# Kernel optimization log

Measured on AMD Instinct MI355X. Metric: run time of the kernel, lower is better.

## Reference

```python
import jax, jax.numpy as jnp
import numpy as np

B, S, DIM = 20, 500, 300          # hard-coded in the original module
HID = 600                          # expansion_factor * dim
QK = 128
ROT = 32                           # rotary dim = min(32, query_key_dim)
NB = 32                            # t5 num_buckets


def _layernorm(x, g, b, eps=1e-5):
    m = jnp.mean(x, -1, keepdims=True)
    v = jnp.var(x, -1, keepdims=True)
    return (x - m) / jnp.sqrt(v + eps) * g + b


def _silu(x):
    return x * jax.nn.sigmoid(x)


def _rotary(x):
    # rotate first ROT dims, adjacent-pair convention (rotary_embedding_torch)
    inv = 1.0 / (10000.0 ** (jnp.arange(0, ROT, 2, dtype=jnp.float32) / ROT))  # [16]
    fr = jnp.repeat(jnp.arange(S, dtype=jnp.float32)[:, None] * inv[None, :], 2, axis=-1)  # [S,32]
    cos, sin = jnp.cos(fr), jnp.sin(fr)
    xr, xp = x[..., :ROT], x[..., ROT:]
    x2 = xr.reshape(xr.shape[0], S, ROT // 2, 2)
    rot = jnp.stack([-x2[..., 1], x2[..., 0]], axis=-1).reshape(xr.shape)
    return jnp.concatenate([xr * cos + rot * sin, xp], axis=-1)


def _t5_bias(emb):
    nb = NB // 2                   # non-causal halves the buckets -> 16
    pos = jnp.arange(S)
    n = pos[:, None] - pos[None, :]  # n = -(k_pos - q_pos)
    ret = (n < 0).astype(jnp.int32) * nb
    na = jnp.abs(n)
    max_exact = nb // 2            # 8
    vil = max_exact + (jnp.log(jnp.maximum(na, 1).astype(jnp.float32) / max_exact)
                       / np.float32(np.log(128.0 / max_exact)) * (nb - max_exact)).astype(jnp.int32)
    vil = jnp.minimum(vil, nb - 1)
    bucket = ret + jnp.where(na < max_exact, na, vil)
    return emb[bucket, 0] * np.float32(QK ** 0.5)


def _gate_mask(gate):
    # Vectorized, jit-able version of the per-batch numpy threshold search.
    T = 128
    absg = jnp.abs(gate)                                   # [B,500,600]
    # histogram of floor(|g|): count(|g|>=t) for integer t via reverse cumsum
    bins = jnp.clip(jnp.floor(absg), 0, T).astype(jnp.int32)
    flat = (bins + (jnp.arange(B, dtype=jnp.int32) * (T + 1))[:, None, None]).ravel()
    hist = jnp.zeros(B * (T + 1), jnp.int32).at[flat].add(1).reshape(B, T + 1)
    cge = jnp.cumsum(hist[:, ::-1], axis=1)[:, ::-1]       # cge[:,t] = #(|g| >= t)
    gmax = jnp.floor(jnp.max(gate, axis=(1, 2)))           # loop starts at floor(max(gate))
    ts = jnp.arange(1, T + 1)
    valid = (ts[None, :] <= gmax[:, None]) & (cge[:, 1:] > 90000)  # 300000*0.3
    trim = jnp.maximum(jnp.max(jnp.where(valid, ts[None, :], 0), axis=1), 1)  # [B]
    g4 = absg.reshape(B, 100, 5, 120, 5)[:, :, :4, :, :4]
    counts = jnp.sum(g4 >= trim[:, None, None, None, None].astype(gate.dtype),
                     axis=(2, 4)).astype(jnp.int32)        # [B,100,120], <=16
    cmax = jnp.max(counts, axis=(1, 2))
    ts2 = jnp.arange(1, 17)
    c2 = jnp.sum(counts[:, :, :, None] >= ts2[None, None, None, :], axis=(1, 2))  # [B,16]
    valid2 = (ts2[None, :] <= cmax[:, None]) & (c2 > 3600)  # 12000*0.3
    found = jnp.any(valid2, axis=1)
    t2 = jnp.where(found, jnp.max(jnp.where(valid2, ts2[None, :], 0), axis=1), cmax)
    bv = jnp.where(counts >= t2[:, None, None], 1.0, 0.25).astype(gate.dtype)  # [B,100,120]
    pr = jnp.array([1.0, 1.0, 1.0, 1.0, 0.0], gate.dtype)  # 5th row/col of each block stays 0
    m = bv[:, :, None, :, None] * pr[None, None, :, None, None] * pr[None, None, None, None, :]
    return m.reshape(B, 500, 600)


def setup_inputs() -> dict:
    key = jax.random.key(0)
    ks = jax.random.split(key, 12)
    std = 0.02
    return {
        "x": jax.random.normal(ks[0], (B, S, DIM), jnp.float32),
        "my_mask2": jax.random.uniform(ks[1], (S, S), jnp.float32),
        "ln_g": jnp.ones((DIM,), jnp.float32),
        "ln_b": jnp.zeros((DIM,), jnp.float32),
        "Wh": jax.random.normal(ks[2], (DIM, 2 * HID), jnp.float32) * std,
        "bh": jnp.zeros((2 * HID,), jnp.float32),
        "Wqk": jax.random.normal(ks[3], (DIM, QK), jnp.float32) * std,
        "bqk": jnp.zeros((QK,), jnp.float32),
        "gamma": 1.0 + jax.random.normal(ks[4], (2, QK), jnp.float32) * std,
        "beta": jnp.zeros((2, QK), jnp.float32),
        "rel_emb": jax.random.normal(ks[5], (NB, 1), jnp.float32) * std,
        "Wout": jax.random.normal(ks[6], (HID, DIM), jnp.float32) * std,
        "bout": jnp.zeros((DIM,), jnp.float32),
    }


def reference(x, my_mask2, ln_g, ln_b, Wh, bh, Wqk, bqk, gamma, beta, rel_emb, Wout, bout):
    nx = _layernorm(x, ln_g, ln_b)
    xs, xp = nx[..., :DIM // 2], nx[..., DIM // 2:]
    xs = jnp.concatenate([jnp.zeros_like(xs[:, :1]), xs[:, :-1]], axis=1)  # token shift
    nx = jnp.concatenate([xs, xp], axis=-1)
    h = _silu(nx @ Wh + bh)                                 # [B,S,1200]
    v, gate = h[..., :HID], h[..., HID:]
    gm = jax.lax.stop_gradient(_gate_mask(gate))            # numpy path detaches in torch
    qk = _silu(nx @ Wqk + bqk)
    q = _rotary(qk * gamma[0] + beta[0])
    k = _rotary(qk * gamma[1] + beta[1])
    sim = jnp.einsum('bid,bjd->bij', q, k) + _t5_bias(rel_emb)[None]
    attn = jax.nn.relu(sim / S) ** 2
    attn = attn * my_mask2[None]
    out = jnp.einsum('bij,bjd->bid', attn, v)
    out = gm * out * gate
    return out @ Wout + bout + x
```

## Files before the change

### kernel.cpp

```cpp
#include <hip/hip_runtime.h>
#include <hip/hip_bf16.h>

#define BB 20
#define SS 500
#define DIMD 300
#define HIDH 600
#define QKD 128

typedef unsigned short u16;
typedef __attribute__((ext_vector_type(8))) __bf16 bf16x8;
typedef __attribute__((ext_vector_type(8))) short short8;
typedef __attribute__((ext_vector_type(4))) float floatx4;

__device__ __forceinline__ u16 f2bu(float f) {
    __hip_bfloat16 h = __float2bfloat16(f);
    return *reinterpret_cast<u16*>(&h);
}
__device__ __forceinline__ float bu2f(u16 u) {
    unsigned v = ((unsigned)u) << 16;
    return __uint_as_float(v);
}

__device__ __forceinline__ floatx4 mfma_bf16(short8 a, short8 b, floatx4 c) {
    return __builtin_amdgcn_mfma_f32_16x16x32_bf16(
        __builtin_bit_cast(bf16x8, a), __builtin_bit_cast(bf16x8, b), c, 0, 0, 0);
}

__device__ __forceinline__ void glds16(const u16* g, u16* l) {
    __builtin_amdgcn_global_load_lds(
        (__attribute__((address_space(1))) const void*)g,
        (__attribute__((address_space(3))) void*)l, 16, 0, 0);
}

__device__ __forceinline__ unsigned fenc(float m) {
    unsigned bits = __float_as_uint(m);
    return (bits & 0x80000000u) ? ~bits : (bits | 0x80000000u);
}

__global__ __launch_bounds__(256)
void prep_ln_kernel(const float* __restrict__ x, const float* __restrict__ lng,
                    const float* __restrict__ lnb, u16* __restrict__ nxb,
                    const float* __restrict__ Wh, const float* __restrict__ Wqk,
                    const float* __restrict__ Wout, const float* __restrict__ rel_emb,
                    u16* __restrict__ WhT, u16* __restrict__ Wqkb,
                    u16* __restrict__ WoutT, float* __restrict__ bias,
                    int* __restrict__ hist, unsigned* __restrict__ gmaxu,
                    int* __restrict__ h2cm) {
    long id = (long)blockIdx.x * 256 + threadIdx.x;
    if (id < 640000) {
        int bs = id >> 6;
        int t = id & 63;
        int s = bs % SS;
        const float* xr = x + (long)bs * DIMD;
        float sum = 0.f, sq = 0.f;
        for (int d = t; d < DIMD; d += 64) { float v = xr[d]; sum += v; sq += v * v; }
        for (int off = 1; off < 64; off <<= 1) {
            sum += __shfl_xor(sum, off);
            sq  += __shfl_xor(sq, off);
        }
        float mean = sum * (1.f / DIMD);
        float var  = sq * (1.f / DIMD) - mean * mean;
        float rstd = rsqrtf(var + 1e-5f);
        for (int d = t; d < DIMD; d += 64) {
            float nv = (xr[d] - mean) * rstd * lng[d] + lnb[d];
            if (d < DIMD / 2) {
                if (s < SS - 1) nxb[(long)(bs + 1) * 320 + d] = f2bu(nv);
            } else {
                nxb[(long)bs * 320 + d] = f2bu(nv);
            }
        }
        if (s == 0)
            for (int d = t; d < DIMD / 2; d += 64) nxb[(long)bs * 320 + d] = 0;
        for (int d = DIMD + t; d < 320; d += 64) nxb[(long)bs * 320 + d] = 0;
        return;
    }
    id -= 640000;
    if (id < 384000) {
        int k = id / 1200, n = id - (long)k * 1200;
        WhT[(long)n * 320 + k] = (k < 300) ? f2bu(Wh[(long)k * 1200 + n]) : (u16)0;
        return;
    }
    id -= 384000;
    if (id < 40960) {
        int k = id / 128, n = id - (long)k * 128;
        Wqkb[(long)n * 320 + k] = (k < 300) ? f2bu(Wqk[(long)k * 128 + n]) : (u16)0;
        return;
    }
    id -= 40960;
    if (id < 182400) {
        int k = id / 300, n = id - (long)k * 300;
        WoutT[(long)n * 608 + k] = (k < 600) ? f2bu(Wout[(long)k * 300 + n]) : (u16)0;
        return;
    }
    id -= 182400;
    if (id < 250000) {
        int i = id / 500, j = id - (long)i * 500;
        int n = i - j;
        int ret = (n < 0) ? 16 : 0;
        int na = n < 0 ? -n : n;
        int bucket;
        if (na < 8) bucket = ret + na;
        else {
            int vil = 8 + (int)(logf((float)na * 0.125f) / logf(16.f) * 8.f);
            vil = vil < 15 ? vil : 15;
            bucket = ret + vil;
        }
        bias[id] = rel_emb[bucket] * 11.313708498984761f;
        return;
    }
    id -= 250000;
    if (id < 5120) { hist[id] = 0; return; }
    id -= 5120;
    if (id < 1280) { gmaxu[id] = 0u; return; }
    id -= 1280;
    if (id < 1280) h2cm[(int)id] = 0;
}


struct EpiH {
    const float* bh; u16* vT; float* gateT; int* hist; unsigned* gmaxu;
    float gm0 = -1e30f, gm1 = -1e30f;
    __device__ void init(int) {}
    __device__ void operator()(float acc, int bz, int m, int n, int j) {
        if (m >= 1200 || n >= 10000) return;
        float v = acc + bh[m];
        v = v / (1.f + expf(-v));
        int b = n / SS, s = n - b * SS;
        if (m < HIDH) { vT[((long)b * 640 + m) * 512 + s] = f2bu(v); return; }
        gateT[((long)b * HIDH + (m - HIDH)) * SS + s] = v;
        if (j) gm1 = fmaxf(gm1, v); else gm0 = fmaxf(gm0, v);
        float ag = fabsf(v);
        if (ag >= 1.f) {
            int bin = (int)fminf(floorf(ag), 128.f);
            atomicAdd(&hist[b * 256 + bin], 1);
        }
    }
    __device__ void flushS(float m, int base) {
        if (base >= 10000) return;
        m = fmaxf(m, __shfl_xor(m, 16));
        m = fmaxf(m, __shfl_xor(m, 32));
        int b0 = base / SS;
        if (b0 == (base + 15) / SS) {
            m = fmaxf(m, __shfl_xor(m, 1));
            m = fmaxf(m, __shfl_xor(m, 2));
            m = fmaxf(m, __shfl_xor(m, 4));
            m = fmaxf(m, __shfl_xor(m, 8));
            if ((threadIdx.x & 63) == 0 && m > -1e29f)
                atomicMax(&gmaxu[b0 * 64], fenc(m));
        } else {
            int l = threadIdx.x & 63;
            if (l < 16 && m > -1e29f)
                atomicMax(&gmaxu[((base + l) / SS) * 64], fenc(m));
        }
    }
    __device__ void finish(int bz, int m0, int n0) {
        if (m0 + 32 <= 600) return;
        flushS(gm0, n0);
        flushS(gm1, n0 + 16);
    }
};
struct EpiQKRot {
    const float* bqk; const float* gamma; const float* beta;
    u16* qb; u16* kb;
    __device__ void init(int) const {}
    __device__ void operator()(float acc, int bz, int m, int n, int j) const {
        float v = acc + bqk[n];
        v = v / (1.f + expf(-v));
        float qp = v * gamma[n] + beta[n];
        float kp = v * gamma[QKD + n] + beta[QKD + n];
        float qx = __shfl_xor(qp, 1);
        float kx = __shfl_xor(kp, 1);
        float qo = qp, ko = kp;
        if (n < 32) {
            int s = m % SS;
            float inv = expf(-(float)(n & ~1) * (logf(10000.f) / 32.f));
            float ang = (float)s * inv;
            float c, sn;
            sincosf(ang, &sn, &c);
            float qr = (n & 1) ? qx : -qx;
            float kr = (n & 1) ? kx : -kx;
            qo = qp * c + qr * sn;
            ko = kp * c + kr * sn;
        }
        if (m < 10000) {
            qb[(long)m * QKD + n] = f2bu(qo);
            kb[(long)m * QKD + n] = f2bu(ko);
        }
    }
    __device__ void finish(int, int, int) const {}
};
struct EpiAttnB {
    const float* bias; const float* mask; u16* attnb;
    __device__ void init(int) const {}
    __device__ void operator()(float acc, int b, int m, int n, int j) const {
        if (m >= SS || n >= 512) return;
        float r = 0.f;
        if (n < SS) {
            float s = (acc + bias[m * SS + n]) * (1.f / (float)SS);
            s = fmaxf(s, 0.f);
            r = s * s * mask[m * SS + n];
        }
        attnb[((long)b * SS + m) * 512 + n] = f2bu(r);
    }
    __device__ void finish(int, int, int) const {}
};
struct EpiGateN {
    const float* gateT; const int* counts; const int* h2cm; u16* gated;
    int t2 = 0;
    __device__ void init(int b) {
        int cmax = h2cm[640 + b * 32];
        int suffix = 0, best = 0;
        bool found = false;
        for (int tt = 16; tt >= 1; --tt) {
            suffix += h2cm[b * 32 + tt];
            if (!found && tt <= cmax && suffix > 3600) { best = tt; found = true; }
        }
        t2 = found ? best : cmax;
    }
    __device__ void operator()(float acc, int b, int m, int n, int j) const {
        if (m >= SS || n >= 608) return;
        float r = 0.f;
        if (n < HIDH) {
            float g = gateT[((long)b * HIDH + n) * SS + m];
            int c = counts[(b * 100 + m / 5) * 120 + n / 5];
            float bv = (c >= t2) ? 1.f : 0.25f;
            float p = ((m % 5) == 4 || (n % 5) == 4) ? 0.f : 1.f;
            r = acc * g * bv * p;
        }
        gated[((long)(b * SS + m)) * 608 + n] = f2bu(r);
    }
    __device__ void finish(int, int, int) const {}
};
struct EpiOutB {
    const float* bout; const float* x; float* out;
    __device__ void init(int) const {}
    __device__ void operator()(float acc, int b, int m, int n, int j) const {
        if (m >= 10000 || n >= DIMD) return;
        out[(long)m * DIMD + n] = acc + bout[n] + x[(long)m * DIMD + n];
    }
    __device__ void finish(int, int, int) const {}
};

template<int MODE, class Epi>
__device__ __forceinline__ void gemm_body(
        int lin, u16* __restrict__ S,
        const u16* __restrict__ A, const u16* __restrict__ Bt,
        int Kp, int lda, int ldb, long sA, long sB,
        int TX, int TY, int bound, Epi epi) {
    int xcd = lin & 7, i = lin >> 3;
    int per = TX * TY;
    int w = i / per;
    int tl = i - w * per;
    int g = xcd + (w << 3);
    int tx = tl % TX, ty = tl / TX;
    int bx, by, bz;
    if (MODE == 0)      { if (g >= bound) return; bx = tx; by = ty; bz = g; }
    else if (MODE == 1) { bx = g * TX + tx; if (bx >= bound) return; by = ty; bz = 0; }
    else                { by = g * TY + ty; if (by >= bound) return; bx = tx; bz = 0; }

    A += (long)bz * sA; Bt += (long)bz * sB;
    int t = threadIdx.x, lane = t & 63, wave = t >> 6;
    int l15 = lane & 15, l4 = lane >> 4;
    int m0 = (by << 6) + ((wave >> 1) << 5);
    int n0 = (bx << 6) + ((wave & 1) << 5);

    epi.init(bz);

    u16* SW = S + (wave << 12);

    int srow = lane >> 2, scol = (lane & 3) << 3;
    const u16* agp0 = A + (long)(m0 + srow) * lda + scol;
    const u16* agp1 = A + (long)(m0 + 16 + srow) * lda + scol;
    const u16* bgp0 = Bt + (long)(n0 + srow) * ldb + scol;
    const u16* bgp1 = Bt + (long)(n0 + 16 + srow) * ldb + scol;

    floatx4 acc[2][2];
#pragma unroll
    for (int i2 = 0; i2 < 2; ++i2)
#pragma unroll
        for (int j = 0; j < 2; ++j) acc[i2][j] = (floatx4){0.f, 0.f, 0.f, 0.f};

    glds16(agp0, SW + 0 * 32);
    glds16(agp1, SW + 16 * 32);
    glds16(bgp0, SW + 32 * 32);
    glds16(bgp1, SW + 48 * 32);

    for (int k0 = 0; k0 < Kp; k0 += 32) {
        int buf = (k0 >> 5) & 1;
        u16* SB = SW + (buf << 11);
        int kn = k0 + 32;
        if (kn < Kp) {
            u16* SN = SW + ((buf ^ 1) << 11);
            glds16(agp0 + kn, SN + 0 * 32);
            glds16(agp1 + kn, SN + 16 * 32);
            glds16(bgp0 + kn, SN + 32 * 32);
            glds16(bgp1 + kn, SN + 48 * 32);
            asm volatile("s_waitcnt vmcnt(4)" ::: "memory");
        } else {
            asm volatile("s_waitcnt vmcnt(0)" ::: "memory");
        }
        short8 a0 = *(const short8*)(SB + l15 * 32 + (l4 << 3));
        short8 a1 = *(const short8*)(SB + (16 + l15) * 32 + (l4 << 3));
        short8 b0 = *(const short8*)(SB + (32 + l15) * 32 + (l4 << 3));
        short8 b1 = *(const short8*)(SB + (48 + l15) * 32 + (l4 << 3));
        acc[0][0] = mfma_bf16(a0, b0, acc[0][0]);
        acc[0][1] = mfma_bf16(a0, b1, acc[0][1]);
        acc[1][0] = mfma_bf16(a1, b0, acc[1][0]);
        acc[1][1] = mfma_bf16(a1, b1, acc[1][1]);
    }
#pragma unroll
    for (int i2 = 0; i2 < 2; ++i2) {
        int bm = m0 + (i2 << 4) + (l4 << 2);
#pragma unroll
        for (int j = 0; j < 2; ++j) {
            int bn = n0 + (j << 4) + l15;
#pragma unroll
            for (int r = 0; r < 4; ++r)
                epi(acc[i2][j][r], bz, bm + r, bn, j);
        }
    }
    epi.finish(bz, m0, n0);
}

template<int MODE, class Epi>
__global__ __launch_bounds__(256)
void gemm_nb(const u16* __restrict__ A, const u16* __restrict__ Bt,
             int Kp, int lda, int ldb, long sA, long sB,
             int TX, int TY, int bound, Epi epi) {
    __shared__ __align__(16) u16 S[4 * 4096];
    gemm_body<MODE>(blockIdx.x, S, A, Bt, Kp, lda, ldb, sA, sB, TX, TY, bound, epi);
}

__global__ __launch_bounds__(256)
void gemm_qk_h(const u16* __restrict__ nxb, const u16* __restrict__ Wqkb,
               const u16* __restrict__ WhT, EpiQKRot eq, EpiH eh) {
    extern __shared__ u16 S[];
    int lin = blockIdx.x;
    if (lin < 320)
        gemm_body<2>(lin, S, nxb, Wqkb, 320, 320, 320, 0L, 0L, 2, 20, 157, eq);
    else
        gemm_body<1>(lin - 320, S, WhT, nxb, 320, 320, 320, 0L, 0L, 20, 19, 157, eh);
}

__global__ __launch_bounds__(256)
void gemm_sc(const u16* __restrict__ qb, const u16* __restrict__ kb, EpiAttnB ea,
             const float* __restrict__ gateT, const int* __restrict__ hist,
             const unsigned* __restrict__ gmaxu, int* __restrict__ counts,
             int* __restrict__ h2cm) {
    extern __shared__ u16 S[];
    int lin = blockIdx.x;
    if (lin < 1536) {
        gemm_body<0>(lin, S, qb, kb, QKD, QKD, QKD,
                     (long)SS * QKD, (long)SS * QKD, 8, 8, BB, ea);
        return;
    }
    int cb = lin - 1536;
    int b = cb / 47, blk = cb - b * 47;
    int r = blk * 256 + threadIdx.x;
    int* h2l = (int*)S;
    int* smaxp = h2l + 17;
    if (threadIdx.x < 17) h2l[threadIdx.x] = 0;
    if (threadIdx.x == 0) *smaxp = 0;
    __syncthreads();
    int c = 0;
    if (r < 12000) {
        unsigned enc = gmaxu[b * 64];
        unsigned bits = (enc & 0x80000000u) ? (enc & 0x7FFFFFFFu) : ~enc;
        float gmax = floorf(__uint_as_float(bits));
        int suffix = 0, trim = 1;
        for (int tt = 128; tt >= 1; --tt) {
            suffix += hist[b * 256 + tt];
            if ((float)tt <= gmax && suffix > 90000) { trim = tt; break; }
        }
        float tr = (float)trim;
        int bi = r / 120, bj = r - bi * 120;
        const float* gb = gateT + (long)b * SS * HIDH;
#pragma unroll
        for (int cc = 0; cc < 4; ++cc)
#pragma unroll
            for (int rr = 0; rr < 4; ++rr) {
                float gv = gb[(long)(bj * 5 + cc) * SS + bi * 5 + rr];
                c += (fabsf(gv) >= tr) ? 1 : 0;
            }
        counts[b * 12000 + r] = c;
        if (c) atomicAdd(&h2l[c], 1);
    }
    int lmax = c;
    for (int off = 32; off; off >>= 1) {
        int o = __shfl_xor(lmax, off);
        lmax = lmax > o ? lmax : o;
    }
    if ((threadIdx.x & 63) == 0) atomicMax(smaxp, lmax);
    __syncthreads();
    if (threadIdx.x < 17 && h2l[threadIdx.x])
        atomicAdd(&h2cm[b * 32 + threadIdx.x], h2l[threadIdx.x]);
    if (threadIdx.x == 0) atomicMax(&h2cm[640 + b * 32], *smaxp);
}

extern "C" void kernel_launch(void* const* d_in, const int* in_sizes, int n_in,
                              void* d_out, int out_size, void* d_ws, size_t ws_size,
                              hipStream_t stream) {
    const float* x      = (const float*)d_in[0];
    const float* mask2  = (const float*)d_in[1];
    const float* ln_g   = (const float*)d_in[2];
    const float* ln_b   = (const float*)d_in[3];
    const float* Wh     = (const float*)d_in[4];
    const float* bh     = (const float*)d_in[5];
    const float* Wqk    = (const float*)d_in[6];
    const float* bqk    = (const float*)d_in[7];
    const float* gamma  = (const float*)d_in[8];
    const float* beta   = (const float*)d_in[9];
    const float* rel_emb= (const float*)d_in[10];
    const float* Wout   = (const float*)d_in[11];
    const float* bout   = (const float*)d_in[12];
    float* out = (float*)d_out;
    float* ws  = (float*)d_ws;

    float* gateT  = ws;
    float* bias   = ws + 6000000;
    u16*   nxb    = (u16*)(ws + 6250000);
    u16*   WhT    = (u16*)(ws + 7850000);
    u16*   Wqkb   = (u16*)(ws + 8042000);
    u16*   WoutT  = (u16*)(ws + 8062480);
    u16*   qb     = (u16*)(ws + 8153680);
    u16*   kb     = (u16*)(ws + 8793680);
    u16*   attnb  = (u16*)(ws + 9433680);
    u16*   vT     = (u16*)(ws + 11993680);
    u16*   gatedb = (u16*)(ws + 15270480);
    int*   hist   = (int*)(ws + 21310480);
    unsigned* gmaxu = (unsigned*)(ws + 21315600);
    int*   counts = (int*)(ws + 21316880);
    int*   h2cm   = (int*)(ws + 21556880);

    prep_ln_kernel<<<5880, 256, 0, stream>>>(x, ln_g, ln_b, nxb, Wh, Wqk, Wout,
                                             rel_emb, WhT, Wqkb, WoutT, bias,
                                             hist, gmaxu, h2cm);

    gemm_qk_h<<<3360, 256, 32768, stream>>>(
        nxb, Wqkb, WhT,
        EpiQKRot{bqk, gamma, beta, qb, kb},
        EpiH{bh, vT, gateT, hist, gmaxu});

    gemm_sc<<<2476, 256, 32768, stream>>>(
        qb, kb, EpiAttnB{bias, mask2, attnb},
        gateT, hist, gmaxu, counts, h2cm);

    gemm_nb<0><<<8 * 10 * 8 * 3, 256, 0, stream>>>(
        attnb, vT, 512, 512, 512,
        (long)SS * 512, (long)640 * 512, 10, 8, BB,
        EpiGateN{gateT, counts, h2cm, gatedb});

    gemm_nb<2><<<8 * 5 * 20, 256, 0, stream>>>(
        gatedb, WoutT, 608, 608, 608, 0L, 0L, 5, 20, 157, EpiOutB{bout, x, out});
}
```

Measured before the change: 229.2 us.

## Share GEMM operand tiles across waves via block-level LDS triple buffering

```diff
diff --git a/kernel.cpp b/kernel.cpp
--- a/kernel.cpp
+++ b/kernel.cpp
@@ -261,18 +261,26 @@
     A += (long)bz * sA; Bt += (long)bz * sB;
     int t = threadIdx.x, lane = t & 63, wave = t >> 6;
     int l15 = lane & 15, l4 = lane >> 4;
-    int m0 = (by << 6) + ((wave >> 1) << 5);
-    int n0 = (bx << 6) + ((wave & 1) << 5);
+    int mw = (wave >> 1) << 5, nw = (wave & 1) << 5;
+    int m0 = (by << 6) + mw;
+    int n0 = (bx << 6) + nw;
 
     epi.init(bz);
 
-    u16* SW = S + (wave << 12);
-
     int srow = lane >> 2, scol = (lane & 3) << 3;
-    const u16* agp0 = A + (long)(m0 + srow) * lda + scol;
-    const u16* agp1 = A + (long)(m0 + 16 + srow) * lda + scol;
-    const u16* bgp0 = Bt + (long)(n0 + srow) * ldb + scol;
-    const u16* bgp1 = Bt + (long)(n0 + 16 + srow) * ldb + scol;
+    const u16* gp0;
+    int drow;
+    if (wave < 2) {
+        gp0 = A + (long)((by << 6) + (wave << 5) + srow) * lda + scol;
+        gp0 += 0;
+        drow = wave << 5;
+    } else {
+        gp0 = Bt + (long)((bx << 6) + ((wave - 2) << 5) + srow) * ldb + scol;
+        drow = 64 + ((wave - 2) << 5);
+    }
+    const u16* gp1 = gp0 + (long)16 * (wave < 2 ? lda : ldb);
+    u16* d0 = S + drow * 32;
+    u16* d1 = S + (drow + 16) * 32;
 
     floatx4 acc[2][2];
 #pragma unroll
@@ -280,33 +288,38 @@
 #pragma unroll
         for (int j = 0; j < 2; ++j) acc[i2][j] = (floatx4){0.f, 0.f, 0.f, 0.f};
 
-    glds16(agp0, SW + 0 * 32);
-    glds16(agp1, SW + 16 * 32);
-    glds16(bgp0, SW + 32 * 32);
-    glds16(bgp1, SW + 48 * 32);
-
-    for (int k0 = 0; k0 < Kp; k0 += 32) {
-        int buf = (k0 >> 5) & 1;
-        u16* SB = SW + (buf << 11);
-        int kn = k0 + 32;
+    int nsteps = Kp >> 5;
+    glds16(gp0, d0);
+    glds16(gp1, d1);
+    if (nsteps > 1) {
+        glds16(gp0 + 32, d0 + 4096);
+        glds16(gp1 + 32, d1 + 4096);
+    }
+
+    int bufc = 0;
+    for (int si = 0; si < nsteps; ++si) {
+        if (si + 1 < nsteps)
+            asm volatile("s_waitcnt vmcnt(2) lgkmcnt(0)" ::: "memory");
+        else
+            asm volatile("s_waitcnt vmcnt(0) lgkmcnt(0)" ::: "memory");
+        __builtin_amdgcn_s_barrier();
+        asm volatile("" ::: "memory");
+        int kn = (si + 2) << 5;
         if (kn < Kp) {
-            u16* SN = SW + ((buf ^ 1) << 11);
-            glds16(agp0 + kn, SN + 0 * 32);
-            glds16(agp1 + kn, SN + 16 * 32);
-            glds16(bgp0 + kn, SN + 32 * 32);
-            glds16(bgp1 + kn, SN + 48 * 32);
-            asm volatile("s_waitcnt vmcnt(4)" ::: "memory");
-        } else {
-            asm volatile("s_waitcnt vmcnt(0)" ::: "memory");
-        }
-        short8 a0 = *(const short8*)(SB + l15 * 32 + (l4 << 3));
-        short8 a1 = *(const short8*)(SB + (16 + l15) * 32 + (l4 << 3));
-        short8 b0 = *(const short8*)(SB + (32 + l15) * 32 + (l4 << 3));
-        short8 b1 = *(const short8*)(SB + (48 + l15) * 32 + (l4 << 3));
+            int bufp = (bufc == 0) ? 2 : bufc - 1;
+            glds16(gp0 + kn, d0 + bufp * 4096);
+            glds16(gp1 + kn, d1 + bufp * 4096);
+        }
+        const u16* SB = S + bufc * 4096;
+        short8 a0 = *(const short8*)(SB + ((mw + l15) << 5) + (l4 << 3));
+        short8 a1 = *(const short8*)(SB + ((mw + 16 + l15) << 5) + (l4 << 3));
+        short8 b0 = *(const short8*)(SB + ((64 + nw + l15) << 5) + (l4 << 3));
+        short8 b1 = *(const short8*)(SB + ((64 + nw + 16 + l15) << 5) + (l4 << 3));
         acc[0][0] = mfma_bf16(a0, b0, acc[0][0]);
         acc[0][1] = mfma_bf16(a0, b1, acc[0][1]);
         acc[1][0] = mfma_bf16(a1, b0, acc[1][0]);
         acc[1][1] = mfma_bf16(a1, b1, acc[1][1]);
+        bufc = (bufc == 2) ? 0 : bufc + 1;
     }
 #pragma unroll
     for (int i2 = 0; i2 < 2; ++i2) {
@@ -327,7 +340,7 @@
 void gemm_nb(const u16* __restrict__ A, const u16* __restrict__ Bt,
              int Kp, int lda, int ldb, long sA, long sB,
              int TX, int TY, int bound, Epi epi) {
-    __shared__ __align__(16) u16 S[4 * 4096];
+    __shared__ __align__(16) u16 S[3 * 4096];
     gemm_body<MODE>(blockIdx.x, S, A, Bt, Kp, lda, ldb, sA, sB, TX, TY, bound, epi);
 }
 
@@ -436,12 +449,12 @@
                                              rel_emb, WhT, Wqkb, WoutT, bias,
                                              hist, gmaxu, h2cm);
 
-    gemm_qk_h<<<3360, 256, 32768, stream>>>(
+    gemm_qk_h<<<3360, 256, 24576, stream>>>(
         nxb, Wqkb, WhT,
         EpiQKRot{bqk, gamma, beta, qb, kb},
         EpiH{bh, vT, gateT, hist, gmaxu});
 
-    gemm_sc<<<2476, 256, 32768, stream>>>(
+    gemm_sc<<<2476, 256, 24576, stream>>>(
         qb, kb, EpiAttnB{bias, mask2, attnb},
         gateT, hist, gmaxu, counts, h2cm);
 
```

New measurement: 212.0 us. 7.5% less time.

## Load MFMA operands directly from global memory, dropping LDS double buffering

Applied to the files above, without the earlier changes.

```diff
diff --git a/kernel.cpp b/kernel.cpp
--- a/kernel.cpp
+++ b/kernel.cpp
@@ -24,12 +24,6 @@
 __device__ __forceinline__ floatx4 mfma_bf16(short8 a, short8 b, floatx4 c) {
     return __builtin_amdgcn_mfma_f32_16x16x32_bf16(
         __builtin_bit_cast(bf16x8, a), __builtin_bit_cast(bf16x8, b), c, 0, 0, 0);
-}
-
-__device__ __forceinline__ void glds16(const u16* g, u16* l) {
-    __builtin_amdgcn_global_load_lds(
-        (__attribute__((address_space(1))) const void*)g,
-        (__attribute__((address_space(3))) void*)l, 16, 0, 0);
 }
 
 __device__ __forceinline__ unsigned fenc(float m) {
@@ -241,11 +235,11 @@
     __device__ void finish(int, int, int) const {}
 };
 
-template<int MODE, class Epi>
+template<int MODE, int NSTEPS, class Epi>
 __device__ __forceinline__ void gemm_body(
-        int lin, u16* __restrict__ S,
+        int lin,
         const u16* __restrict__ A, const u16* __restrict__ Bt,
-        int Kp, int lda, int ldb, long sA, long sB,
+        int lda, int ldb, long sA, long sB,
         int TX, int TY, int bound, Epi epi) {
     int xcd = lin & 7, i = lin >> 3;
     int per = TX * TY;
@@ -266,13 +260,10 @@
 
     epi.init(bz);
 
-    u16* SW = S + (wave << 12);
-
-    int srow = lane >> 2, scol = (lane & 3) << 3;
-    const u16* agp0 = A + (long)(m0 + srow) * lda + scol;
-    const u16* agp1 = A + (long)(m0 + 16 + srow) * lda + scol;
-    const u16* bgp0 = Bt + (long)(n0 + srow) * ldb + scol;
-    const u16* bgp1 = Bt + (long)(n0 + 16 + srow) * ldb + scol;
+    const u16* ap0 = A + (long)(m0 + l15) * lda + (l4 << 3);
+    const u16* ap1 = ap0 + (long)16 * lda;
+    const u16* bp0 = Bt + (long)(n0 + l15) * ldb + (l4 << 3);
+    const u16* bp1 = bp0 + (long)16 * ldb;
 
     floatx4 acc[2][2];
 #pragma unroll
@@ -280,29 +271,12 @@
 #pragma unroll
         for (int j = 0; j < 2; ++j) acc[i2][j] = (floatx4){0.f, 0.f, 0.f, 0.f};
 
-    glds16(agp0, SW + 0 * 32);
-    glds16(agp1, SW + 16 * 32);
-    glds16(bgp0, SW + 32 * 32);
-    glds16(bgp1, SW + 48 * 32);
-
-    for (int k0 = 0; k0 < Kp; k0 += 32) {
-        int buf = (k0 >> 5) & 1;
-        u16* SB = SW + (buf << 11);
-        int kn = k0 + 32;
-        if (kn < Kp) {
-            u16* SN = SW + ((buf ^ 1) << 11);
-            glds16(agp0 + kn, SN + 0 * 32);
-            glds16(agp1 + kn, SN + 16 * 32);
-            glds16(bgp0 + kn, SN + 32 * 32);
-            glds16(bgp1 + kn, SN + 48 * 32);
-            asm volatile("s_waitcnt vmcnt(4)" ::: "memory");
-        } else {
-            asm volatile("s_waitcnt vmcnt(0)" ::: "memory");
-        }
-        short8 a0 = *(const short8*)(SB + l15 * 32 + (l4 << 3));
-        short8 a1 = *(const short8*)(SB + (16 + l15) * 32 + (l4 << 3));
-        short8 b0 = *(const short8*)(SB + (32 + l15) * 32 + (l4 << 3));
-        short8 b1 = *(const short8*)(SB + (48 + l15) * 32 + (l4 << 3));
+#pragma unroll
+    for (int s = 0; s < NSTEPS; ++s) {
+        short8 a0 = *(const short8*)(ap0 + (s << 5));
+        short8 a1 = *(const short8*)(ap1 + (s << 5));
+        short8 b0 = *(const short8*)(bp0 + (s << 5));
+        short8 b1 = *(const short8*)(bp1 + (s << 5));
         acc[0][0] = mfma_bf16(a0, b0, acc[0][0]);
         acc[0][1] = mfma_bf16(a0, b1, acc[0][1]);
         acc[1][0] = mfma_bf16(a1, b0, acc[1][0]);
@@ -322,45 +296,41 @@
     epi.finish(bz, m0, n0);
 }
 
-template<int MODE, class Epi>
-__global__ __launch_bounds__(256)
+template<int MODE, int NSTEPS, class Epi>
+__global__ __launch_bounds__(256, 4)
 void gemm_nb(const u16* __restrict__ A, const u16* __restrict__ Bt,
-             int Kp, int lda, int ldb, long sA, long sB,
+             int lda, int ldb, long sA, long sB,
              int TX, int TY, int bound, Epi epi) {
-    __shared__ __align__(16) u16 S[4 * 4096];
-    gemm_body<MODE>(blockIdx.x, S, A, Bt, Kp, lda, ldb, sA, sB, TX, TY, bound, epi);
-}
-
-__global__ __launch_bounds__(256)
+    gemm_body<MODE, NSTEPS>(blockIdx.x, A, Bt, lda, ldb, sA, sB, TX, TY, bound, epi);
+}
+
+__global__ __launch_bounds__(256, 4)
 void gemm_qk_h(const u16* __restrict__ nxb, const u16* __restrict__ Wqkb,
                const u16* __restrict__ WhT, EpiQKRot eq, EpiH eh) {
-    extern __shared__ u16 S[];
     int lin = blockIdx.x;
     if (lin < 320)
-        gemm_body<2>(lin, S, nxb, Wqkb, 320, 320, 320, 0L, 0L, 2, 20, 157, eq);
+        gemm_body<2, 10>(lin, nxb, Wqkb, 320, 320, 0L, 0L, 2, 20, 157, eq);
     else
-        gemm_body<1>(lin - 320, S, WhT, nxb, 320, 320, 320, 0L, 0L, 20, 19, 157, eh);
-}
-
-__global__ __launch_bounds__(256)
+        gemm_body<1, 10>(lin - 320, WhT, nxb, 320, 320, 0L, 0L, 20, 19, 157, eh);
+}
+
+__global__ __launch_bounds__(256, 4)
 void gemm_sc(const u16* __restrict__ qb, const u16* __restrict__ kb, EpiAttnB ea,
              const float* __restrict__ gateT, const int* __restrict__ hist,
              const unsigned* __restrict__ gmaxu, int* __restrict__ counts,
              int* __restrict__ h2cm) {
-    extern __shared__ u16 S[];
+    __shared__ int h2l[18];
     int lin = blockIdx.x;
     if (lin < 1536) {
-        gemm_body<0>(lin, S, qb, kb, QKD, QKD, QKD,
-                     (long)SS * QKD, (long)SS * QKD, 8, 8, BB, ea);
+        gemm_body<0, 4>(lin, qb, kb, QKD, QKD,
+                        (long)SS * QKD, (long)SS * QKD, 8, 8, BB, ea);
         return;
     }
     int cb = lin - 1536;
     int b = cb / 47, blk = cb - b * 47;
     int r = blk * 256 + threadIdx.x;
-    int* h2l = (int*)S;
-    int* smaxp = h2l + 17;
     if (threadIdx.x < 17) h2l[threadIdx.x] = 0;
-    if (threadIdx.x == 0) *smaxp = 0;
+    if (threadIdx.x == 0) h2l[17] = 0;
     __syncthreads();
     int c = 0;
     if (r < 12000) {
@@ -390,11 +360,11 @@
         int o = __shfl_xor(lmax, off);
         lmax = lmax > o ? lmax : o;
     }
-    if ((threadIdx.x & 63) == 0) atomicMax(smaxp, lmax);
+    if ((threadIdx.x & 63) == 0) atomicMax(&h2l[17], lmax);
     __syncthreads();
     if (threadIdx.x < 17 && h2l[threadIdx.x])
         atomicAdd(&h2cm[b * 32 + threadIdx.x], h2l[threadIdx.x]);
-    if (threadIdx.x == 0) atomicMax(&h2cm[640 + b * 32], *smaxp);
+    if (threadIdx.x == 0) atomicMax(&h2cm[640 + b * 32], h2l[17]);
 }
 
 extern "C" void kernel_launch(void* const* d_in, const int* in_sizes, int n_in,
@@ -436,20 +406,20 @@
                                              rel_emb, WhT, Wqkb, WoutT, bias,
                                              hist, gmaxu, h2cm);
 
-    gemm_qk_h<<<3360, 256, 32768, stream>>>(
+    gemm_qk_h<<<3360, 256, 0, stream>>>(
         nxb, Wqkb, WhT,
         EpiQKRot{bqk, gamma, beta, qb, kb},
         EpiH{bh, vT, gateT, hist, gmaxu});
 
-    gemm_sc<<<2476, 256, 32768, stream>>>(
+    gemm_sc<<<2476, 256, 0, stream>>>(
         qb, kb, EpiAttnB{bias, mask2, attnb},
         gateT, hist, gmaxu, counts, h2cm);
 
-    gemm_nb<0><<<8 * 10 * 8 * 3, 256, 0, stream>>>(
-        attnb, vT, 512, 512, 512,
+    gemm_nb<0, 16><<<8 * 10 * 8 * 3, 256, 0, stream>>>(
+        attnb, vT, 512, 512,
         (long)SS * 512, (long)640 * 512, 10, 8, BB,
         EpiGateN{gateT, counts, h2cm, gatedb});
 
-    gemm_nb<2><<<8 * 5 * 20, 256, 0, stream>>>(
-        gatedb, WoutT, 608, 608, 608, 0L, 0L, 5, 20, 157, EpiOutB{bout, x, out});
-}
+    gemm_nb<2, 19><<<8 * 5 * 20, 256, 0, stream>>>(
+        gatedb, WoutT, 608, 608, 0L, 0L, 5, 20, 157, EpiOutB{bout, x, out});
+}
```

Result: slower. 306.3 us (+33.6%).
